# Kernel tuning notes

Hardware: AMD Instinct MI355X
Metric: run time of the kernel (lower is better)

The kernel has to match this reference:

```python
import jax, jax.numpy as jnp
import numpy as np

B, T, C = 2, 2048, 2048
H, Hk, D = 32, 4, 64
N_REP = H // Hk
THETA = 10000.0


def _rope_tables():
    inv_freq = 1.0 / (THETA ** (np.arange(0, D, 2, dtype=np.float64) / D))  # [D/2]
    t = np.arange(T, dtype=np.float64)
    freqs = np.outer(t, inv_freq)                # [T, D/2]
    emb = np.repeat(freqs, 2, axis=-1)           # interleaved [T, D]
    return jnp.asarray(np.cos(emb), jnp.float32), jnp.asarray(np.sin(emb), jnp.float32)


def setup_inputs() -> dict:
    key = jax.random.key(0)
    kx, kq, kk, kv, ko = jax.random.split(key, 5)
    scale = 0.02
    x = jax.random.normal(kx, (B, T, C), jnp.float32)
    wq = jax.random.normal(kq, (H * D, C), jnp.float32) * scale
    wk = jax.random.normal(kk, (Hk * D, C), jnp.float32) * scale
    wv = jax.random.normal(kv, (Hk * D, C), jnp.float32) * scale
    wo = jax.random.normal(ko, (C, H * D), jnp.float32) * scale
    cos, sin = _rope_tables()
    return {"x": x, "cos": cos, "sin": sin, "wq": wq, "wk": wk, "wv": wv, "wo": wo}


def _apply_rope(x, cos, sin):
    # x: [B, h, T, D]; cos/sin: [T, D] interleaved
    x1 = x[..., 0::2]
    x2 = x[..., 1::2]
    rot = jnp.stack([-x2, x1], axis=-1).reshape(x.shape)
    return x * cos[None, None] + rot * sin[None, None]


def reference(x, cos, sin, wq, wk, wv, wo):
    q = (x @ wq.T).reshape(B, T, H, D).transpose(0, 2, 1, 3)    # [B,H,T,D]
    k = (x @ wk.T).reshape(B, T, Hk, D).transpose(0, 2, 1, 3)   # [B,Hk,T,D]
    v = (x @ wv.T).reshape(B, T, Hk, D).transpose(0, 2, 1, 3)   # [B,Hk,T,D]
    q = _apply_rope(q, cos, sin)
    k = _apply_rope(k, cos, sin)
    # new_cache = (k, v) pre-repeat
    kr = jnp.repeat(k, N_REP, axis=1)                            # [B,H,T,D]
    vr = jnp.repeat(v, N_REP, axis=1)
    scores = jnp.einsum('bhtd,bhsd->bhts', q, kr) / jnp.sqrt(jnp.float32(D))
    mask = jnp.tril(jnp.ones((T, T), dtype=bool))                # causal (kv_cache is None)
    scores = jnp.where(mask, scores, jnp.finfo(scores.dtype).min)
    attn = jax.nn.softmax(scores, axis=-1)
    o = jnp.einsum('bhts,bhsd->bhtd', attn, vr)
    o = o.transpose(0, 2, 1, 3).reshape(B, T, H * D)
    return (o @ wo.T, k, v)
```

## Files before the change

kernel.cpp:

```cpp
#include <hip/hip_runtime.h>
#include <hip/hip_bf16.h>

#define B_ 2
#define T_ 2048
#define C_ 2048
#define H_ 32
#define HK_ 4
#define D_ 64

typedef __attribute__((ext_vector_type(4)))  float f32x4;
typedef __attribute__((ext_vector_type(2)))  float f32x2;
typedef __attribute__((ext_vector_type(16))) float f32x16;
typedef __attribute__((ext_vector_type(8)))  short bf16x8;

static __device__ __forceinline__ unsigned short f2bf(float f) {
  union { __hip_bfloat16 h; unsigned short s; } u;
  u.h = __float2bfloat16(f);
  return u.s;
}
static __device__ __forceinline__ float bf2f(unsigned short s) {
  union { unsigned int u; float f; } u; u.u = ((unsigned int)s) << 16; return u.f;
}
static __device__ __forceinline__ unsigned int cvtpk(float lo, float hi) {
  unsigned int r;
  asm("v_cvt_pk_bf16_f32 %0, %1, %2" : "=v"(r) : "v"(lo), "v"(hi));
  return r;
}

#define GLD16(gp, lp) __builtin_amdgcn_global_load_lds( \
    (const __attribute__((address_space(1))) unsigned int*)(gp), \
    (__attribute__((address_space(3))) unsigned int*)(unsigned int)(uintptr_t)(lp), 16, 0, 0)

__global__ void f32_to_bf16(const float* __restrict__ src, unsigned short* __restrict__ dst, int n4) {
  const int i = blockIdx.x * blockDim.x + threadIdx.x;
  if (i >= n4) return;
  f32x4 v = *(const f32x4*)(src + 4 * (size_t)i);
  ushort4 o;
  o.x = f2bf(v[0]); o.y = f2bf(v[1]); o.z = f2bf(v[2]); o.w = f2bf(v[3]);
  *(ushort4*)(dst + 4 * (size_t)i) = o;
}

template<int EPI>
__global__ __launch_bounds__(256, 2)
void gemm128(const unsigned short* __restrict__ A, const unsigned short* __restrict__ W,
             int M, int N, int K,
             float* __restrict__ Cf,
             const float* __restrict__ cosT, const float* __restrict__ sinT,
             unsigned short* __restrict__ qb, unsigned short* __restrict__ kbf,
             unsigned short* __restrict__ vtb, float* __restrict__ koutf,
             float* __restrict__ voutf) {
  __shared__ unsigned short As[2][128 * 64];
  __shared__ unsigned short Bs[2][128 * 64];

  const int tid  = threadIdx.x;
  const int lane = tid & 63;
  const int w    = tid >> 6;
  const int wm   = w >> 1, wn = w & 1;
  const int g    = lane >> 4;
  const int lr   = lane & 15;

  const int bm = blockIdx.y * 128;
  const int bn = blockIdx.x * 128;

  const int sr8 = lane >> 3;
  const int sch = (lane & 7) ^ sr8;
  const unsigned short* Ag = A + (size_t)(bm + w * 8 + sr8) * K + sch * 8;
  const unsigned short* Wg = W + (size_t)(bn + w * 8 + sr8) * K + sch * 8;

#define STG(buf, k0) do { \
    GLD16(Ag + (k0),                   &As[buf][(     w * 8) * 64]); \
    GLD16(Ag + (size_t)32  * K + (k0), &As[buf][(32 + w * 8) * 64]); \
    GLD16(Ag + (size_t)64  * K + (k0), &As[buf][(64 + w * 8) * 64]); \
    GLD16(Ag + (size_t)96  * K + (k0), &As[buf][(96 + w * 8) * 64]); \
    GLD16(Wg + (k0),                   &Bs[buf][(     w * 8) * 64]); \
    GLD16(Wg + (size_t)32  * K + (k0), &Bs[buf][(32 + w * 8) * 64]); \
    GLD16(Wg + (size_t)64  * K + (k0), &Bs[buf][(64 + w * 8) * 64]); \
    GLD16(Wg + (size_t)96  * K + (k0), &Bs[buf][(96 + w * 8) * 64]); \
  } while (0)

  f32x4 acc[4][4] = {};
  const int nt = K >> 6;
  STG(0, 0);

  for (int t = 0; t < nt; ++t) {
    const int p = t & 1;
    asm volatile("s_waitcnt vmcnt(0)" ::: "memory");
    __builtin_amdgcn_s_barrier();
    if (t + 1 < nt) STG(p ^ 1, (t + 1) << 6);

    const unsigned short* At = &As[p][0];
    const unsigned short* Bt = &Bs[p][0];
#pragma unroll
    for (int kh = 0; kh < 2; ++kh) {
      bf16x8 af[4], wf[4];
#pragma unroll
      for (int m = 0; m < 4; m++) {
        const int row = wm * 64 + m * 16 + lr;
        af[m] = *(const bf16x8*)&At[row * 64 + (((g + 4 * kh) ^ (row & 7)) << 3)];
      }
#pragma unroll
      for (int n = 0; n < 4; n++) {
        const int row = wn * 64 + n * 16 + lr;
        wf[n] = *(const bf16x8*)&Bt[row * 64 + (((g + 4 * kh) ^ (row & 7)) << 3)];
      }
      __builtin_amdgcn_s_setprio(1);
#pragma unroll
      for (int m = 0; m < 4; m++)
#pragma unroll
        for (int n = 0; n < 4; n++)
          acc[m][n] = __builtin_amdgcn_mfma_f32_16x16x32_bf16(af[m], wf[n], acc[m][n], 0, 0, 0);
      __builtin_amdgcn_s_setprio(0);
    }
  }
#undef STG

  if (EPI == 0) {
#pragma unroll
    for (int m = 0; m < 4; m++) {
      const int row = bm + wm * 64 + m * 16 + g * 4;
#pragma unroll
      for (int n = 0; n < 4; n++) {
        const int col = bn + wn * 64 + n * 16 + lr;
#pragma unroll
        for (int r = 0; r < 4; r++)
          Cf[(size_t)(row + r) * N + col] = acc[m][n][r];
      }
    }
  } else {
    const int seg = (bn < 2048) ? 0 : (bn < 2304 ? 1 : 2);
#pragma unroll
    for (int m = 0; m < 4; m++) {
#pragma unroll
      for (int n = 0; n < 4; n++) {
        const int col = bn + wn * 64 + n * 16 + lr;
        const int d   = col & 63;
#pragma unroll
        for (int r = 0; r < 4; r++) {
          const int row = bm + wm * 64 + m * 16 + g * 4 + r;
          const int tt  = row & (T_ - 1);
          const int bb  = row >> 11;
          const float val = acc[m][n][r];
          if (seg == 2) {
            const int hk = (col >> 6) - 36;
            const size_t idx = ((size_t)(bb * HK_ + hk) * T_ + tt) * D_ + d;
            voutf[idx] = val;
            const int tm   = tt & 15;
            const int tpos = (tt & ~15) | ((tm & 3) + ((tm >> 3) << 2) + ((tm & 4) << 1));
            vtb[((size_t)(bb * HK_ + hk) * D_ + d) * T_ + tpos] = f2bf(val);
          } else {
            const float cs = cosT[tt * D_ + d];
            const float sn = sinT[tt * D_ + d];
            const float other = __shfl_xor(val, 1);
            const float o = val * cs + ((lr & 1) ? other : -other) * sn;
            if (seg == 0) {
              const int h = col >> 6;
              qb[((size_t)(bb * H_ + h) * T_ + tt) * D_ + d] = f2bf(o);
            } else {
              const int hk = (col >> 6) - 32;
              const size_t idx = ((size_t)(bb * HK_ + hk) * T_ + tt) * D_ + d;
              koutf[idx] = o;
              kbf[idx]   = f2bf(o);
            }
          }
        }
      }
    }
  }
}

__global__ __launch_bounds__(512, 4)
void gqa_attn4(const unsigned short* __restrict__ qb,
               const unsigned short* __restrict__ kb,
               const unsigned short* __restrict__ vt,
               unsigned short* __restrict__ ob) {
  __shared__ unsigned short Ks[3][4096];
  __shared__ unsigned short Vs[3][4096];

  const int tid  = threadIdx.x;
  const int lane = tid & 63;
  const int w    = tid >> 6;
  const int qi   = lane & 31;
  const int hi   = lane >> 5;

  const int qt = 63 - (int)(blockIdx.x >> 3);
  const int go = blockIdx.x & 7;
  const int b  = go >> 2;
  const int hk = go & 3;
  const int h  = hk * 8 + w;
  const int bh = b * H_ + h;

  const int qbase = qt * 32;
  const int qrow  = qbase + qi;

  const unsigned short* qptr = qb + ((size_t)bh * T_ + qrow) * D_ + 8 * hi;
  bf16x8 qf[4];
#pragma unroll
  for (int c = 0; c < 4; c++) qf[c] = *(const bf16x8*)(qptr + 16 * c);

  const int srow   = lane >> 3;
  const int schunk = (lane & 7) ^ srow;
  const int krow   = 8 * w + srow;
  const unsigned short* gK = kb + (size_t)(b * HK_ + hk) * T_ * D_ + (size_t)krow * D_ + schunk * 8;
  const unsigned short* gV = vt + (size_t)(b * HK_ + hk) * D_ * T_ + (size_t)krow * T_ + schunk * 8;
  unsigned short* ldsK = &Ks[0][w * 512];
  unsigned short* ldsV = &Vs[0][w * 512];

#define STAGE_KV(pp, kk0) do { \
    GLD16(gK + (size_t)(kk0) * D_, ldsK + (pp) * 4096); \
    GLD16(gV + (kk0),              ldsV + (pp) * 4096); \
  } while (0)

  f32x16 o0 = {}, o1 = {};
  float m = -1e30f, l = 0.f;
  float c1 = 0.f;
  const float SC   = 0.125f * 1.44269504089f;
  const float THRR = 44.3614195f;
  const int   swz  = qi & 7;

  const int nt = ((qbase + 31) >> 6) + 1;
  STAGE_KV(0, 0);
  if (nt > 1) STAGE_KV(1, 64);

  int p = 0;
  for (int it = 0; it < nt; ++it) {
    const int kb0 = it * 64;
    const bool last = (it == nt - 1);
    const bool has1 = (kb0 + 32 <= qbase + 31);

    asm volatile("s_waitcnt lgkmcnt(0)" ::: "memory");
    if (it + 1 < nt) asm volatile("s_waitcnt vmcnt(2)" ::: "memory");
    else             asm volatile("s_waitcnt vmcnt(0)" ::: "memory");
    asm volatile("s_barrier" ::: "memory");
    if (it + 2 < nt) STAGE_KV((p + 2 > 2) ? p - 1 : p + 2, kb0 + 128);

    const unsigned short* Kt = &Ks[0][0] + p * 4096;
    const unsigned short* Vt = &Vs[0][0] + p * 4096;

    f32x16 st0 = {}, st1 = {};
    __builtin_amdgcn_s_setprio(1);
#pragma unroll
    for (int c = 0; c < 4; c++) {
      bf16x8 kf = *(const bf16x8*)&Kt[qi * 64 + (((hi + 2 * c) ^ swz) << 3)];
      st0 = __builtin_amdgcn_mfma_f32_32x32x16_bf16(kf, qf[c], st0, 0, 0, 0);
    }
    if (!last || has1) {
#pragma unroll
      for (int c = 0; c < 4; c++) {
        bf16x8 kf = *(const bf16x8*)&Kt[(32 + qi) * 64 + (((hi + 2 * c) ^ swz) << 3)];
        st1 = __builtin_amdgcn_mfma_f32_32x32x16_bf16(kf, qf[c], st1, 0, 0, 0);
      }
    }
    __builtin_amdgcn_s_setprio(0);

    if (last) {
#pragma unroll
      for (int r = 0; r < 16; ++r) {
        const int key = kb0 + (r & 3) + 8 * (r >> 2) + 4 * hi;
        st0[r] = (key      <= qrow) ? st0[r] : -1e30f;
        st1[r] = (key + 32 <= qrow) ? st1[r] : -1e30f;
      }
    }

    float tmax = fmaxf(st0[0], st0[1]);
#pragma unroll
    for (int r = 2; r < 16; ++r) tmax = fmaxf(tmax, st0[r]);
#pragma unroll
    for (int r = 0; r < 16; ++r) tmax = fmaxf(tmax, st1[r]);
    tmax = fmaxf(tmax, __shfl_xor(tmax, 32));

    if (!__all(tmax <= m + THRR)) {
      const float mnew  = fmaxf(m, tmax);
      const float al    = __builtin_amdgcn_exp2f((m - mnew) * SC);
#pragma unroll
      for (int r = 0; r < 16; ++r) { o0[r] *= al; o1[r] *= al; }
      l *= al;
      m  = mnew;
      c1 = -m * SC;
    }

    float sum = 0.f;
#pragma unroll
    for (int r = 0; r < 16; ++r) { float pv = __builtin_amdgcn_exp2f(__builtin_fmaf(st0[r], SC, c1)); st0[r] = pv; sum += pv; }
#pragma unroll
    for (int r = 0; r < 16; ++r) { float pv = __builtin_amdgcn_exp2f(__builtin_fmaf(st1[r], SC, c1)); st1[r] = pv; sum += pv; }
    sum += __shfl_xor(sum, 32);
    l += sum;

    union U8 { bf16x8 v; unsigned int u[4]; };
    U8 pf[4];
#pragma unroll
    for (int j = 0; j < 4; ++j) {
      pf[0].u[j] = cvtpk(st0[2 * j],     st0[2 * j + 1]);
      pf[1].u[j] = cvtpk(st0[8 + 2 * j], st0[8 + 2 * j + 1]);
      pf[2].u[j] = cvtpk(st1[2 * j],     st1[2 * j + 1]);
      pf[3].u[j] = cvtpk(st1[8 + 2 * j], st1[8 + 2 * j + 1]);
    }

    const int ncf = (!last || has1) ? 4 : 2;
    __builtin_amdgcn_s_setprio(1);
#pragma unroll
    for (int dh = 0; dh < 2; ++dh) {
      const unsigned short* Vrow = &Vt[(dh * 32 + qi) * 64];
      f32x16 oc = dh ? o1 : o0;
#pragma unroll
      for (int c = 0; c < 4; ++c) {
        if (c >= ncf) break;
        bf16x8 vf = *(const bf16x8*)&Vrow[(((2 * c + hi) ^ swz) << 3)];
        oc = __builtin_amdgcn_mfma_f32_32x32x16_bf16(vf, pf[c].v, oc, 0, 0, 0);
      }
      if (dh) o1 = oc; else o0 = oc;
    }
    __builtin_amdgcn_s_setprio(0);

    p = (p > 1) ? 0 : p + 1;
  }

  const float inv = 1.0f / l;
  unsigned short* orow = ob + (size_t)(b * T_ + qrow) * (H_ * D_) + h * D_;
#pragma unroll
  for (int dh = 0; dh < 2; ++dh) {
    const f32x16 ov = dh ? o1 : o0;
#pragma unroll
    for (int rg = 0; rg < 4; ++rg) {
      const int d0 = 32 * dh + 8 * rg + 4 * hi;
      ushort4 pk;
      pk.x = f2bf(ov[4 * rg + 0] * inv);
      pk.y = f2bf(ov[4 * rg + 1] * inv);
      pk.z = f2bf(ov[4 * rg + 2] * inv);
      pk.w = f2bf(ov[4 * rg + 3] * inv);
      *(ushort4*)(orow + d0) = pk;
    }
  }
#undef STAGE_KV
}

extern "C" void kernel_launch(void* const* d_in, const int* in_sizes, int n_in,
                              void* d_out, int out_size, void* d_ws, size_t ws_size,
                              hipStream_t stream) {
  const float* x    = (const float*)d_in[0];
  const float* cosT = (const float*)d_in[1];
  const float* sinT = (const float*)d_in[2];
  const float* wq   = (const float*)d_in[3];
  const float* wk   = (const float*)d_in[4];
  const float* wv   = (const float*)d_in[5];
  const float* wo   = (const float*)d_in[6];

  float* y    = (float*)d_out;
  float* kout = (float*)d_out + (size_t)B_ * T_ * C_;
  float* vout = kout + (size_t)B_ * HK_ * T_ * D_;

  char* ws = (char*)d_ws;
  unsigned short* x_bf = (unsigned short*)(ws);
  unsigned short* o_bf = x_bf;
  unsigned short* wqkv = (unsigned short*)(ws + 16777216);
  unsigned short* q_bf = (unsigned short*)(ws + 27262976);
  unsigned short* k_bf = (unsigned short*)(ws + 44040192);
  unsigned short* v_t  = (unsigned short*)(ws + 46137344);
  unsigned short* wo_bf= (unsigned short*)(ws + 48234496);

  const int M = B_ * T_;

  f32_to_bf16<<<8192, 256, 0, stream>>>(x,  x_bf, 2097152);
  f32_to_bf16<<<4096, 256, 0, stream>>>(wq, wqkv,               1048576);
  f32_to_bf16<<<512,  256, 0, stream>>>(wk, wqkv + 2048 * 2048, 131072);
  f32_to_bf16<<<512,  256, 0, stream>>>(wv, wqkv + 2304 * 2048, 131072);
  f32_to_bf16<<<4096, 256, 0, stream>>>(wo, wo_bf,              1048576);

  gemm128<1><<<dim3(2560 / 128, M / 128), 256, 0, stream>>>(
      x_bf, wqkv, M, 2560, C_, nullptr, cosT, sinT, q_bf, k_bf, v_t, kout, vout);

  gqa_attn4<<<512, 512, 0, stream>>>(q_bf, k_bf, v_t, o_bf);

  gemm128<0><<<dim3(C_ / 128, M / 128), 256, 0, stream>>>(
      o_bf, wo_bf, M, C_, H_ * D_, y, nullptr, nullptr, nullptr, nullptr, nullptr, nullptr, nullptr);
}
```

Baseline: 198.7 us.

## Replace 128x128 GEMM with 256x256 8-wave ping-pong pipelined GEMM

Swaps the 4-wave 128x128 double-buffered GEMM for an 8-wave 256x256 tile kernel that uses 128KB of dynamic LDS. Each K step is split into four MFMA phases separated by barriers, and loads for the next stages are interleaved between them. The goal is more data reuse per tile and better overlap of global-to-LDS loads with MFMA work. The risk is that the grid shrinks: the QKV GEMM now launches 10x16 = 160 blocks and the output GEMM 8x16 = 128 blocks, which is fewer than the number of CUs on MI355X, so part of the GPU may sit idle.

```diff
diff --git a/kernel.cpp b/kernel.cpp
--- a/kernel.cpp
+++ b/kernel.cpp
@@ -30,6 +30,8 @@
 #define GLD16(gp, lp) __builtin_amdgcn_global_load_lds( \
     (const __attribute__((address_space(1))) unsigned int*)(gp), \
     (__attribute__((address_space(3))) unsigned int*)(unsigned int)(uintptr_t)(lp), 16, 0, 0)
+
+#define BAR() asm volatile("s_barrier" ::: "memory")
 
 __global__ void f32_to_bf16(const float* __restrict__ src, unsigned short* __restrict__ dst, int n4) {
   const int i = blockIdx.x * blockDim.x + threadIdx.x;
@@ -40,106 +42,156 @@
   *(ushort4*)(dst + 4 * (size_t)i) = o;
 }
 
+static __device__ __forceinline__ void mm16(f32x4 (&acc)[8][4], const bf16x8 (&a)[4][2],
+                                            const bf16x8 (&b)[2][2], const int mh, const int nb) {
+  __builtin_amdgcn_s_setprio(1);
+#pragma unroll
+  for (int m = 0; m < 4; m++)
+#pragma unroll
+    for (int n = 0; n < 2; n++)
+#pragma unroll
+      for (int kh = 0; kh < 2; kh++)
+        acc[mh * 4 + m][nb + n] =
+            __builtin_amdgcn_mfma_f32_16x16x32_bf16(a[m][kh], b[n][kh], acc[mh * 4 + m][nb + n], 0, 0, 0);
+  __builtin_amdgcn_s_setprio(0);
+}
+
 template<int EPI>
-__global__ __launch_bounds__(256, 2)
-void gemm128(const unsigned short* __restrict__ A, const unsigned short* __restrict__ W,
-             int M, int N, int K,
-             float* __restrict__ Cf,
-             const float* __restrict__ cosT, const float* __restrict__ sinT,
-             unsigned short* __restrict__ qb, unsigned short* __restrict__ kbf,
-             unsigned short* __restrict__ vtb, float* __restrict__ koutf,
-             float* __restrict__ voutf) {
-  __shared__ unsigned short As[2][128 * 64];
-  __shared__ unsigned short Bs[2][128 * 64];
+__global__ __launch_bounds__(512, 2)
+void gemm8p(const unsigned short* __restrict__ A, const unsigned short* __restrict__ W,
+            int M, int N, int K,
+            float* __restrict__ Cf,
+            const float* __restrict__ cosT, const float* __restrict__ sinT,
+            unsigned short* __restrict__ qb, unsigned short* __restrict__ kbf,
+            unsigned short* __restrict__ vtb, float* __restrict__ koutf,
+            float* __restrict__ voutf) {
+  extern __shared__ unsigned short lds[];
+#define ASL(buf, h) (lds + (buf) * 16384 + (h) * 8192)
+#define BSL(buf, h) (lds + 32768 + (buf) * 16384 + (h) * 8192)
 
   const int tid  = threadIdx.x;
   const int lane = tid & 63;
   const int w    = tid >> 6;
-  const int wm   = w >> 1, wn = w & 1;
+  const int wm   = w >> 2;
+  const int wn   = w & 3;
   const int g    = lane >> 4;
   const int lr   = lane & 15;
 
-  const int bm = blockIdx.y * 128;
-  const int bn = blockIdx.x * 128;
+  const int bm = blockIdx.y * 256;
+  const int bn = blockIdx.x * 256;
 
   const int sr8 = lane >> 3;
   const int sch = (lane & 7) ^ sr8;
   const unsigned short* Ag = A + (size_t)(bm + w * 8 + sr8) * K + sch * 8;
   const unsigned short* Wg = W + (size_t)(bn + w * 8 + sr8) * K + sch * 8;
 
-#define STG(buf, k0) do { \
-    GLD16(Ag + (k0),                   &As[buf][(     w * 8) * 64]); \
-    GLD16(Ag + (size_t)32  * K + (k0), &As[buf][(32 + w * 8) * 64]); \
-    GLD16(Ag + (size_t)64  * K + (k0), &As[buf][(64 + w * 8) * 64]); \
-    GLD16(Ag + (size_t)96  * K + (k0), &As[buf][(96 + w * 8) * 64]); \
-    GLD16(Wg + (k0),                   &Bs[buf][(     w * 8) * 64]); \
-    GLD16(Wg + (size_t)32  * K + (k0), &Bs[buf][(32 + w * 8) * 64]); \
-    GLD16(Wg + (size_t)64  * K + (k0), &Bs[buf][(64 + w * 8) * 64]); \
-    GLD16(Wg + (size_t)96  * K + (k0), &Bs[buf][(96 + w * 8) * 64]); \
+#define STAGE_A(buf, h, k0) do { \
+    GLD16(Ag + (size_t)((h) * 128     ) * K + (k0), ASL(buf, h) + (     w * 8) * 64); \
+    GLD16(Ag + (size_t)((h) * 128 + 64) * K + (k0), ASL(buf, h) + (64 + w * 8) * 64); \
   } while (0)
-
-  f32x4 acc[4][4] = {};
+#define STAGE_B(buf, h, k0) do { \
+    GLD16(Wg + (size_t)((h) * 128     ) * K + (k0), BSL(buf, h) + (     w * 8) * 64); \
+    GLD16(Wg + (size_t)((h) * 128 + 64) * K + (k0), BSL(buf, h) + (64 + w * 8) * 64); \
+  } while (0)
+
+  f32x4 acc[8][4] = {};
   const int nt = K >> 6;
-  STG(0, 0);
-
-  for (int t = 0; t < nt; ++t) {
-    const int p = t & 1;
-    asm volatile("s_waitcnt vmcnt(0)" ::: "memory");
-    __builtin_amdgcn_s_barrier();
-    if (t + 1 < nt) STG(p ^ 1, (t + 1) << 6);
-
-    const unsigned short* At = &As[p][0];
-    const unsigned short* Bt = &Bs[p][0];
-#pragma unroll
-    for (int kh = 0; kh < 2; ++kh) {
-      bf16x8 af[4], wf[4];
-#pragma unroll
-      for (int m = 0; m < 4; m++) {
-        const int row = wm * 64 + m * 16 + lr;
-        af[m] = *(const bf16x8*)&At[row * 64 + (((g + 4 * kh) ^ (row & 7)) << 3)];
-      }
-#pragma unroll
-      for (int n = 0; n < 4; n++) {
-        const int row = wn * 64 + n * 16 + lr;
-        wf[n] = *(const bf16x8*)&Bt[row * 64 + (((g + 4 * kh) ^ (row & 7)) << 3)];
-      }
-      __builtin_amdgcn_s_setprio(1);
-#pragma unroll
-      for (int m = 0; m < 4; m++)
-#pragma unroll
-        for (int n = 0; n < 4; n++)
-          acc[m][n] = __builtin_amdgcn_mfma_f32_16x16x32_bf16(af[m], wf[n], acc[m][n], 0, 0, 0);
-      __builtin_amdgcn_s_setprio(0);
-    }
+
+  STAGE_A(0, 0, 0); STAGE_A(0, 1, 0);
+  STAGE_B(0, 0, 0); STAGE_B(0, 1, 0);
+  STAGE_B(1, 0, 64); STAGE_B(1, 1, 64);
+  asm volatile("s_waitcnt vmcnt(4)" ::: "memory");
+  BAR();
+
+  for (int U = 0; U < nt; ++U) {
+    const int buf = U & 1, nbuf = buf ^ 1;
+    const int k1 = (U + 1) << 6, k2 = (U + 2) << 6;
+    const unsigned short* Abase = ASL(buf, wm);
+    const unsigned short* Bbase = BSL(buf, wn >> 1);
+
+    bf16x8 a[4][2], b0[2][2], b1[2][2];
+
+#pragma unroll
+    for (int m = 0; m < 4; m++)
+#pragma unroll
+      for (int kh = 0; kh < 2; kh++) {
+        const int row = m * 16 + lr;
+        a[m][kh] = *(const bf16x8*)&Abase[row * 64 + (((kh * 4 + g) ^ (row & 7)) << 3)];
+      }
+#pragma unroll
+    for (int n = 0; n < 2; n++)
+#pragma unroll
+      for (int kh = 0; kh < 2; kh++) {
+        const int row = (wn & 1) * 64 + n * 16 + lr;
+        b0[n][kh] = *(const bf16x8*)&Bbase[row * 64 + (((kh * 4 + g) ^ (row & 7)) << 3)];
+      }
+    if (U + 1 < nt) STAGE_A(nbuf, 0, k1);
+    BAR();
+    mm16(acc, a, b0, 0, 0);
+    BAR();
+
+#pragma unroll
+    for (int n = 0; n < 2; n++)
+#pragma unroll
+      for (int kh = 0; kh < 2; kh++) {
+        const int row = (wn & 1) * 64 + (2 + n) * 16 + lr;
+        b1[n][kh] = *(const bf16x8*)&Bbase[row * 64 + (((kh * 4 + g) ^ (row & 7)) << 3)];
+      }
+    if (U + 1 < nt) STAGE_A(nbuf, 1, k1);
+    BAR();
+    mm16(acc, a, b1, 0, 2);
+    BAR();
+
+#pragma unroll
+    for (int m = 0; m < 4; m++)
+#pragma unroll
+      for (int kh = 0; kh < 2; kh++) {
+        const int row = 64 + m * 16 + lr;
+        a[m][kh] = *(const bf16x8*)&Abase[row * 64 + (((kh * 4 + g) ^ (row & 7)) << 3)];
+      }
+    if (U + 2 < nt) STAGE_B(buf, 0, k2);
+    BAR();
+    mm16(acc, a, b1, 1, 2);
+    BAR();
+
+    if (U + 2 < nt) STAGE_B(buf, 1, k2);
+    BAR();
+    mm16(acc, a, b0, 1, 0);
+    if (U + 2 < nt) asm volatile("s_waitcnt vmcnt(4)" ::: "memory");
+    else            asm volatile("s_waitcnt vmcnt(0)" ::: "memory");
+    BAR();
   }
-#undef STG
+#undef STAGE_A
+#undef STAGE_B
+#undef ASL
+#undef BSL
 
   if (EPI == 0) {
 #pragma unroll
-    for (int m = 0; m < 4; m++) {
-      const int row = bm + wm * 64 + m * 16 + g * 4;
-#pragma unroll
-      for (int n = 0; n < 4; n++) {
-        const int col = bn + wn * 64 + n * 16 + lr;
+    for (int mf = 0; mf < 8; mf++) {
+      const int row = bm + wm * 128 + mf * 16 + g * 4;
+#pragma unroll
+      for (int nf = 0; nf < 4; nf++) {
+        const int col = bn + wn * 64 + nf * 16 + lr;
 #pragma unroll
         for (int r = 0; r < 4; r++)
-          Cf[(size_t)(row + r) * N + col] = acc[m][n][r];
+          Cf[(size_t)(row + r) * N + col] = acc[mf][nf][r];
       }
     }
   } else {
-    const int seg = (bn < 2048) ? 0 : (bn < 2304 ? 1 : 2);
-#pragma unroll
-    for (int m = 0; m < 4; m++) {
-#pragma unroll
-      for (int n = 0; n < 4; n++) {
-        const int col = bn + wn * 64 + n * 16 + lr;
+    const int seg = (bn < 2048) ? 0 : (bn == 2048 ? 1 : 2);
+#pragma unroll
+    for (int mf = 0; mf < 8; mf++) {
+#pragma unroll
+      for (int nf = 0; nf < 4; nf++) {
+        const int col = bn + wn * 64 + nf * 16 + lr;
         const int d   = col & 63;
 #pragma unroll
         for (int r = 0; r < 4; r++) {
-          const int row = bm + wm * 64 + m * 16 + g * 4 + r;
+          const int row = bm + wm * 128 + mf * 16 + g * 4 + r;
           const int tt  = row & (T_ - 1);
           const int bb  = row >> 11;
-          const float val = acc[m][n][r];
+          const float val = acc[mf][nf][r];
           if (seg == 2) {
             const int hk = (col >> 6) - 36;
             const size_t idx = ((size_t)(bb * HK_ + hk) * T_ + tt) * D_ + d;
@@ -360,17 +412,20 @@
 
   const int M = B_ * T_;
 
+  (void)hipFuncSetAttribute((const void*)gemm8p<0>, hipFuncAttributeMaxDynamicSharedMemorySize, 131072);
+  (void)hipFuncSetAttribute((const void*)gemm8p<1>, hipFuncAttributeMaxDynamicSharedMemorySize, 131072);
+
   f32_to_bf16<<<8192, 256, 0, stream>>>(x,  x_bf, 2097152);
   f32_to_bf16<<<4096, 256, 0, stream>>>(wq, wqkv,               1048576);
   f32_to_bf16<<<512,  256, 0, stream>>>(wk, wqkv + 2048 * 2048, 131072);
   f32_to_bf16<<<512,  256, 0, stream>>>(wv, wqkv + 2304 * 2048, 131072);
   f32_to_bf16<<<4096, 256, 0, stream>>>(wo, wo_bf,              1048576);
 
-  gemm128<1><<<dim3(2560 / 128, M / 128), 256, 0, stream>>>(
+  gemm8p<1><<<dim3(2560 / 256, M / 256), 512, 131072, stream>>>(
       x_bf, wqkv, M, 2560, C_, nullptr, cosT, sinT, q_bf, k_bf, v_t, kout, vout);
 
   gqa_attn4<<<512, 512, 0, stream>>>(q_bf, k_bf, v_t, o_bf);
 
-  gemm128<0><<<dim3(C_ / 128, M / 128), 256, 0, stream>>>(
+  gemm8p<0><<<dim3(C_ / 256, M / 256), 512, 131072, stream>>>(
       o_bf, wo_bf, M, C_, H_ * D_, y, nullptr, nullptr, nullptr, nullptr, nullptr, nullptr, nullptr);
 }
```

New measurement: 217.9 us. 1.1x slower.

## Triple-buffer GEMM with BK=32 pipeline and XCD-aware block swizzle

Applied to the files above, without the earlier changes.

Reworks the projection GEMM to a three-stage shared-memory ring with 32-wide K tiles, prefetching two tiles ahead and waiting with a partial vmcnt so loads overlap compute. LDS per block shrinks, so launch bounds are raised to three blocks per CU. Block indices are remapped so consecutive tiles spread across the chiplets in groups of eight. It costs twice as many barriers per K step and finer-grained loads, and the remap assumes the grid divides evenly by eight.

```diff
diff --git a/kernel.cpp b/kernel.cpp
--- a/kernel.cpp
+++ b/kernel.cpp
@@ -41,16 +41,16 @@
 }
 
 template<int EPI>
-__global__ __launch_bounds__(256, 2)
-void gemm128(const unsigned short* __restrict__ A, const unsigned short* __restrict__ W,
-             int M, int N, int K,
-             float* __restrict__ Cf,
-             const float* __restrict__ cosT, const float* __restrict__ sinT,
-             unsigned short* __restrict__ qb, unsigned short* __restrict__ kbf,
-             unsigned short* __restrict__ vtb, float* __restrict__ koutf,
-             float* __restrict__ voutf) {
-  __shared__ unsigned short As[2][128 * 64];
-  __shared__ unsigned short Bs[2][128 * 64];
+__global__ __launch_bounds__(256, 3)
+void gemm3(const unsigned short* __restrict__ A, const unsigned short* __restrict__ W,
+           int M, int N, int K,
+           float* __restrict__ Cf,
+           const float* __restrict__ cosT, const float* __restrict__ sinT,
+           unsigned short* __restrict__ qb, unsigned short* __restrict__ kbf,
+           unsigned short* __restrict__ vtb, float* __restrict__ koutf,
+           float* __restrict__ voutf) {
+  __shared__ unsigned short As[3][128 * 32];
+  __shared__ unsigned short Ws[3][128 * 32];
 
   const int tid  = threadIdx.x;
   const int lane = tid & 63;
@@ -59,60 +59,64 @@
   const int g    = lane >> 4;
   const int lr   = lane & 15;
 
-  const int bm = blockIdx.y * 128;
-  const int bn = blockIdx.x * 128;
-
-  const int sr8 = lane >> 3;
-  const int sch = (lane & 7) ^ sr8;
-  const unsigned short* Ag = A + (size_t)(bm + w * 8 + sr8) * K + sch * 8;
-  const unsigned short* Wg = W + (size_t)(bn + w * 8 + sr8) * K + sch * 8;
-
-#define STG(buf, k0) do { \
-    GLD16(Ag + (k0),                   &As[buf][(     w * 8) * 64]); \
-    GLD16(Ag + (size_t)32  * K + (k0), &As[buf][(32 + w * 8) * 64]); \
-    GLD16(Ag + (size_t)64  * K + (k0), &As[buf][(64 + w * 8) * 64]); \
-    GLD16(Ag + (size_t)96  * K + (k0), &As[buf][(96 + w * 8) * 64]); \
-    GLD16(Wg + (k0),                   &Bs[buf][(     w * 8) * 64]); \
-    GLD16(Wg + (size_t)32  * K + (k0), &Bs[buf][(32 + w * 8) * 64]); \
-    GLD16(Wg + (size_t)64  * K + (k0), &Bs[buf][(64 + w * 8) * 64]); \
-    GLD16(Wg + (size_t)96  * K + (k0), &Bs[buf][(96 + w * 8) * 64]); \
+  const int gx   = gridDim.x;
+  const int flat = blockIdx.y * gx + blockIdx.x;
+  const int cpx  = (gx * gridDim.y) >> 3;
+  const int swzb = (flat & 7) * cpx + (flat >> 3);
+  const int bm   = (swzb / gx) * 128;
+  const int bn   = (swzb % gx) * 128;
+
+  const int srow = tid >> 2;
+  const int sc   = (tid & 3) ^ (srow & 3);
+  const unsigned short* Ag = A + (size_t)(bm + srow) * K + sc * 8;
+  const unsigned short* Wg = W + (size_t)(bn + srow) * K + sc * 8;
+
+#define STAGE3(buf, k0) do { \
+    GLD16(Ag + (k0),                  &As[buf][       w * 512]); \
+    GLD16(Ag + (size_t)64 * K + (k0), &As[buf][2048 + w * 512]); \
+    GLD16(Wg + (k0),                  &Ws[buf][       w * 512]); \
+    GLD16(Wg + (size_t)64 * K + (k0), &Ws[buf][2048 + w * 512]); \
   } while (0)
 
   f32x4 acc[4][4] = {};
-  const int nt = K >> 6;
-  STG(0, 0);
+
+  const int nt = K >> 5;
+  STAGE3(0, 0);
+  STAGE3(1, 32);
 
   for (int t = 0; t < nt; ++t) {
-    const int p = t & 1;
-    asm volatile("s_waitcnt vmcnt(0)" ::: "memory");
-    __builtin_amdgcn_s_barrier();
-    if (t + 1 < nt) STG(p ^ 1, (t + 1) << 6);
-
-    const unsigned short* At = &As[p][0];
-    const unsigned short* Bt = &Bs[p][0];
-#pragma unroll
-    for (int kh = 0; kh < 2; ++kh) {
-      bf16x8 af[4], wf[4];
-#pragma unroll
-      for (int m = 0; m < 4; m++) {
-        const int row = wm * 64 + m * 16 + lr;
-        af[m] = *(const bf16x8*)&At[row * 64 + (((g + 4 * kh) ^ (row & 7)) << 3)];
-      }
-#pragma unroll
-      for (int n = 0; n < 4; n++) {
-        const int row = wn * 64 + n * 16 + lr;
-        wf[n] = *(const bf16x8*)&Bt[row * 64 + (((g + 4 * kh) ^ (row & 7)) << 3)];
-      }
-      __builtin_amdgcn_s_setprio(1);
-#pragma unroll
-      for (int m = 0; m < 4; m++)
-#pragma unroll
-        for (int n = 0; n < 4; n++)
-          acc[m][n] = __builtin_amdgcn_mfma_f32_16x16x32_bf16(af[m], wf[n], acc[m][n], 0, 0, 0);
-      __builtin_amdgcn_s_setprio(0);
-    }
+    if (t + 1 < nt) asm volatile("s_waitcnt vmcnt(4)" ::: "memory");
+    else            asm volatile("s_waitcnt vmcnt(0)" ::: "memory");
+    asm volatile("s_barrier" ::: "memory");
+
+    if (t + 2 < nt) {
+      const int nb = (t + 2) % 3;
+      STAGE3(nb, (size_t)(t + 2) * 32);
+    }
+
+    const unsigned short* At = &As[t % 3][0];
+    const unsigned short* Wt = &Ws[t % 3][0];
+
+    bf16x8 af[4], wf[4];
+#pragma unroll
+    for (int m = 0; m < 4; m++) {
+      const int row = wm * 64 + m * 16 + lr;
+      af[m] = *(const bf16x8*)&At[row * 32 + ((g ^ (row & 3)) << 3)];
+    }
+#pragma unroll
+    for (int n = 0; n < 4; n++) {
+      const int row = wn * 64 + n * 16 + lr;
+      wf[n] = *(const bf16x8*)&Wt[row * 32 + ((g ^ (row & 3)) << 3)];
+    }
+    __builtin_amdgcn_s_setprio(1);
+#pragma unroll
+    for (int m = 0; m < 4; m++)
+#pragma unroll
+      for (int n = 0; n < 4; n++)
+        acc[m][n] = __builtin_amdgcn_mfma_f32_16x16x32_bf16(af[m], wf[n], acc[m][n], 0, 0, 0);
+    __builtin_amdgcn_s_setprio(0);
   }
-#undef STG
+#undef STAGE3
 
   if (EPI == 0) {
 #pragma unroll
@@ -366,11 +370,11 @@
   f32_to_bf16<<<512,  256, 0, stream>>>(wv, wqkv + 2304 * 2048, 131072);
   f32_to_bf16<<<4096, 256, 0, stream>>>(wo, wo_bf,              1048576);
 
-  gemm128<1><<<dim3(2560 / 128, M / 128), 256, 0, stream>>>(
+  gemm3<1><<<dim3(2560 / 128, M / 128), 256, 0, stream>>>(
       x_bf, wqkv, M, 2560, C_, nullptr, cosT, sinT, q_bf, k_bf, v_t, kout, vout);
 
   gqa_attn4<<<512, 512, 0, stream>>>(q_bf, k_bf, v_t, o_bf);
 
-  gemm128<0><<<dim3(C_ / 128, M / 128), 256, 0, stream>>>(
+  gemm3<0><<<dim3(C_ / 128, M / 128), 256, 0, stream>>>(
       o_bf, wo_bf, M, C_, H_ * D_, y, nullptr, nullptr, nullptr, nullptr, nullptr, nullptr, nullptr);
 }
```

Measured after the change: 196.7 us. No clear change (-1.0%).
